# Performance work log

Measured on AMD Instinct MI355X. Metric: run time of the kernel, lower is better.

The kernel has to match this reference:

```python
import jax, jax.numpy as jnp
import numpy as np

N_NODES = 50000
N_RAND_EDGES = 800000
IN_FEATS = 128
NUM_HEADS = 4
OUT_FEATS = 32
NEG_SLOPE = 0.2


def setup_inputs() -> dict:
    key = jax.random.key(0)
    k_feat, k_src, k_dst, k_w, k_al, k_ar, k_b = jax.random.split(key, 7)
    feat = jax.random.normal(k_feat, (N_NODES, IN_FEATS), dtype=jnp.float32)
    # random edges + self-loops so every node has in-degree >= 1 (DGL requirement)
    src_r = jax.random.randint(k_src, (N_RAND_EDGES,), 0, N_NODES)
    dst_r = jax.random.randint(k_dst, (N_RAND_EDGES,), 0, N_NODES)
    loops = jnp.arange(N_NODES, dtype=src_r.dtype)
    src = jnp.concatenate([src_r, loops]).astype(jnp.int64)
    dst = jnp.concatenate([dst_r, loops]).astype(jnp.int64)
    W = jax.random.normal(k_w, (NUM_HEADS * OUT_FEATS, IN_FEATS), dtype=jnp.float32) * 0.05
    attn_l = jax.random.normal(k_al, (1, NUM_HEADS, OUT_FEATS), dtype=jnp.float32) * 0.1
    attn_r = jax.random.normal(k_ar, (1, NUM_HEADS, OUT_FEATS), dtype=jnp.float32) * 0.1
    bias = jnp.zeros((NUM_HEADS * OUT_FEATS,), dtype=jnp.float32)
    return {"feat": feat, "src": src, "dst": dst, "W": W,
            "attn_l": attn_l, "attn_r": attn_r, "bias": bias}


def _gat_forward(feat, src, dst, W, attn_l, attn_r, bias):
    n = feat.shape[0]
    # shared projection: in homogeneous path feat_src2 = feat_dst2 = fc(h)
    ft = (feat @ W.T).reshape(n, NUM_HEADS, OUT_FEATS)       # [N,H,D]
    el = jnp.sum(ft * attn_l, axis=-1)                        # [N,H]
    er = jnp.sum(ft * attn_r, axis=-1)                        # [N,H]
    e = el[src] + er[dst]                                     # [E,H]
    e = jnp.where(e > 0, e, NEG_SLOPE * e)                    # leaky_relu
    # edge softmax per destination node (numerically stable)
    m = jax.ops.segment_max(e, dst, num_segments=n)           # [N,H]
    ex = jnp.exp(e - m[dst])
    s = jax.ops.segment_sum(ex, dst, num_segments=n)          # [N,H]
    a = ex / s[dst]                                           # [E,H]
    # u_mul_e -> sum : attention-weighted aggregation
    msg1 = ft[src] * a[:, :, None]                            # [E,H,D]
    initial_ft = jax.ops.segment_sum(msg1, dst, num_segments=n)
    # u_mul_v -> sum : elementwise src*dst product aggregation
    msg2 = ft[src] * ft[dst]                                  # [E,H,D]
    add_ft = jax.ops.segment_sum(msg2, dst, num_segments=n)
    rst = initial_ft + add_ft + bias.reshape(1, NUM_HEADS, OUT_FEATS)
    return rst


def reference(feat, src, dst, W, attn_l, attn_r, bias):
    return _gat_forward(feat, src, dst, W, attn_l, attn_r, bias)
```

## Files before the change

kernel.cpp:

```cpp
#include <hip/hip_runtime.h>
#include <hip/hip_bf16.h>

#define IN_FEATS 128
#define HD 128
#define NEG_SLOPE 0.2f
#define LDR 128
#define CAP 64

typedef short s8v __attribute__((ext_vector_type(8)));
typedef float f4v __attribute__((ext_vector_type(4)));

static __device__ __forceinline__ unsigned short f2bf(float f) {
    unsigned int u = __float_as_uint(f);
    unsigned int r = (u + 0x7FFFu + ((u >> 16) & 1u)) >> 16;
    return (unsigned short)r;
}
static __device__ __forceinline__ float bf2f(unsigned short h) {
    return __uint_as_float(((unsigned int)h) << 16);
}

#define GM 64
#define LDA 136
#define SCAT_BLOCKS 512
__global__ __launch_bounds__(256) void scatter_gemm(const float* __restrict__ feat,
                                                    const float* __restrict__ W,
                                                    const float* __restrict__ attn_l,
                                                    const float* __restrict__ attn_r,
                                                    const int* __restrict__ src,
                                                    const int* __restrict__ dst,
                                                    int* __restrict__ cnt,
                                                    int* __restrict__ bucket, int E,
                                                    unsigned short* __restrict__ ftb,
                                                    float* __restrict__ el,
                                                    float* __restrict__ er, int N) {
    if (blockIdx.x < SCAT_BLOCKS) {
        const int gstride = SCAT_BLOCKS * 256;
        for (int i = blockIdx.x * 256 + threadIdx.x; i < E; i += gstride) {
            int d = dst[i];
            int pos = atomicAdd(&cnt[d], 1);
            if (pos < CAP) bucket[((size_t)d << 6) + pos] = src[i];
        }
        return;
    }

    __shared__ unsigned short Wb[128][LDA];
    __shared__ unsigned short Ab[GM][LDA];

    const int tid   = threadIdx.x;
    const int wave  = tid >> 6;
    const int lane  = tid & 63;
    const int m     = lane & 15;
    const int quad  = lane >> 4;
    const int rbase = (blockIdx.x - SCAT_BLOCKS) * GM;

    const float4* W4 = (const float4*)W;
    for (int i = tid; i < 4096; i += 256) {
        int r = i >> 5, q = i & 31;
        float4 w = W4[i];
        ushort4 o;
        o.x = f2bf(w.x); o.y = f2bf(w.y); o.z = f2bf(w.z); o.w = f2bf(w.w);
        *(ushort4*)&Wb[r][q * 4] = o;
    }
    const float4* F4 = (const float4*)feat;
    for (int i = tid; i < 2048; i += 256) {
        int r = i >> 5, q = i & 31;
        int gr = rbase + r;
        float4 v = (gr < N) ? F4[(size_t)gr * 32 + q]
                            : make_float4(0.f, 0.f, 0.f, 0.f);
        ushort4 o;
        o.x = f2bf(v.x); o.y = f2bf(v.y); o.z = f2bf(v.z); o.w = f2bf(v.w);
        *(ushort4*)&Ab[r][q * 4] = o;
    }
    __syncthreads();

    f4v acc[8];
#pragma unroll
    for (int t = 0; t < 8; ++t) acc[t] = (f4v){0.f, 0.f, 0.f, 0.f};

    const int arow = wave * 16 + m;
#pragma unroll
    for (int k0 = 0; k0 < 4; ++k0) {
        s8v a = *(const s8v*)&Ab[arow][k0 * 32 + quad * 8];
#pragma unroll
        for (int t = 0; t < 8; ++t) {
            s8v b = *(const s8v*)&Wb[t * 16 + m][k0 * 32 + quad * 8];
            acc[t] = __builtin_amdgcn_mfma_f32_16x16x32_bf16(a, b, acc[t], 0, 0, 0);
        }
    }

#pragma unroll
    for (int reg = 0; reg < 4; ++reg) {
        int gr = rbase + wave * 16 + quad * 4 + reg;
        if (gr < N) {
            unsigned short* dstrow = &ftb[(size_t)gr * LDR];
#pragma unroll
            for (int t = 0; t < 8; ++t)
                dstrow[t * 16 + m] = f2bf(acc[t][reg]);
        }
    }

    float al[8], ar[8];
#pragma unroll
    for (int t = 0; t < 8; ++t) {
        al[t] = attn_l[t * 16 + m];
        ar[t] = attn_r[t * 16 + m];
    }
#pragma unroll
    for (int h = 0; h < 4; ++h) {
#pragma unroll
        for (int reg = 0; reg < 4; ++reg) {
            float pl = acc[2 * h][reg] * al[2 * h] + acc[2 * h + 1][reg] * al[2 * h + 1];
            float pr = acc[2 * h][reg] * ar[2 * h] + acc[2 * h + 1][reg] * ar[2 * h + 1];
            pl += __shfl_xor(pl, 1); pr += __shfl_xor(pr, 1);
            pl += __shfl_xor(pl, 2); pr += __shfl_xor(pr, 2);
            pl += __shfl_xor(pl, 4); pr += __shfl_xor(pr, 4);
            pl += __shfl_xor(pl, 8); pr += __shfl_xor(pr, 8);
            if (m == 0) {
                int gr = rbase + wave * 16 + quad * 4 + reg;
                if (gr < N) {
                    el[gr * 4 + h] = pl;
                    er[gr * 4 + h] = pr;
                }
            }
        }
    }
}

__global__ __launch_bounds__(256) void aggregate_kernel(
        const unsigned short* __restrict__ ftb, const float* __restrict__ el,
        const float* __restrict__ er, const int* __restrict__ cnt,
        const int* __restrict__ bucket, const float* __restrict__ bias,
        float* __restrict__ out, int N) {
    const int n    = (blockIdx.x * blockDim.x + threadIdx.x) >> 6;
    const int lane = threadIdx.x & 63;
    if (n >= N) return;
    const int h  = lane >> 4;
    const int c0 = lane * 2;

    const float ern = er[(n << 2) + h];
    ushort2 tn = *(const ushort2*)(ftb + (size_t)n * LDR + c0);
    const float ftn0 = bf2f(tn.x), ftn1 = bf2f(tn.y);

    int deg = min(cnt[n], CAP);
    const int* eb = bucket + ((size_t)n << 6);

    float a0 = 0.f, a1 = 0.f;
    float b0 = 0.f, b1 = 0.f;
    float sum = 0.f;

    int i = 0;
    for (; i + 4 <= deg; i += 4) {
        int sA = eb[i + 0], sB = eb[i + 1], sC = eb[i + 2], sD = eb[i + 3];
        float eA = el[(sA << 2) + h];
        float eB = el[(sB << 2) + h];
        float eC = el[(sC << 2) + h];
        float eD = el[(sD << 2) + h];
        ushort2 fA = *(const ushort2*)(ftb + (size_t)sA * LDR + c0);
        ushort2 fB = *(const ushort2*)(ftb + (size_t)sB * LDR + c0);
        ushort2 fC = *(const ushort2*)(ftb + (size_t)sC * LDR + c0);
        ushort2 fD = *(const ushort2*)(ftb + (size_t)sD * LDR + c0);
        eA += ern; eB += ern; eC += ern; eD += ern;
        eA = eA > 0.f ? eA : NEG_SLOPE * eA;
        eB = eB > 0.f ? eB : NEG_SLOPE * eB;
        eC = eC > 0.f ? eC : NEG_SLOPE * eC;
        eD = eD > 0.f ? eD : NEG_SLOPE * eD;
        float xA = __expf(eA), xB = __expf(eB);
        float xC = __expf(eC), xD = __expf(eD);
        float fAx = bf2f(fA.x), fAy = bf2f(fA.y);
        float fBx = bf2f(fB.x), fBy = bf2f(fB.y);
        float fCx = bf2f(fC.x), fCy = bf2f(fC.y);
        float fDx = bf2f(fD.x), fDy = bf2f(fD.y);
        sum += (xA + xB) + (xC + xD);
        a0 += xA * fAx + xB * fBx + xC * fCx + xD * fDx;
        a1 += xA * fAy + xB * fBy + xC * fCy + xD * fDy;
        b0 += (fAx + fBx) + (fCx + fDx);
        b1 += (fAy + fBy) + (fCy + fDy);
    }
    for (; i < deg; ++i) {
        int s = eb[i];
        float e = el[(s << 2) + h] + ern;
        e = e > 0.f ? e : NEG_SLOPE * e;
        float x = __expf(e);
        ushort2 f = *(const ushort2*)(ftb + (size_t)s * LDR + c0);
        float fx = bf2f(f.x), fy = bf2f(f.y);
        sum += x;
        a0 += x * fx; a1 += x * fy;
        b0 += fx;     b1 += fy;
    }

    float inv = 1.f / sum;
    float2 o;
    o.x = a0 * inv + ftn0 * b0 + bias[c0];
    o.y = a1 * inv + ftn1 * b1 + bias[c0 + 1];
    *(float2*)(out + (size_t)n * HD + c0) = o;
}

extern "C" void kernel_launch(void* const* d_in, const int* in_sizes, int n_in,
                              void* d_out, int out_size, void* d_ws, size_t ws_size,
                              hipStream_t stream) {
    const float* feat   = (const float*)d_in[0];
    const int*   src    = (const int*)d_in[1];
    const int*   dst    = (const int*)d_in[2];
    const float* W      = (const float*)d_in[3];
    const float* attn_l = (const float*)d_in[4];
    const float* attn_r = (const float*)d_in[5];
    const float* bias   = (const float*)d_in[6];

    const int N = in_sizes[0] / IN_FEATS;
    const int E = in_sizes[1];

    char* p = (char*)d_ws;
    auto alloc = [&](size_t bytes) {
        char* q = p;
        p += (bytes + 255) & ~(size_t)255;
        return q;
    };
    unsigned short* ftb = (unsigned short*)alloc((size_t)N * LDR * 2);
    float* el    = (float*)alloc((size_t)N * 4 * 4);
    float* er    = (float*)alloc((size_t)N * 4 * 4);
    int*   cnt   = (int*)alloc((size_t)N * 4);
    int*   bucket= (int*)alloc((size_t)N * CAP * 4);

    hipMemsetAsync(cnt, 0, (size_t)N * 4, stream);

    const int gemm_blocks = (N + GM - 1) / GM;
    scatter_gemm<<<SCAT_BLOCKS + gemm_blocks, 256, 0, stream>>>(
        feat, W, attn_l, attn_r, src, dst, cnt, bucket, E, ftb, el, er, N);

    long long threads = (long long)N * 64;
    int agg_blocks = (int)((threads + 255) / 256);
    aggregate_kernel<<<agg_blocks, 256, 0, stream>>>(ftb, el, er, cnt, bucket,
                                                     bias, (float*)d_out, N);
}
```

Before: 195.7 us.

## Load W fragments directly from global, pack bf16 pairs, unroll scatter by two

```diff
diff --git a/kernel.cpp b/kernel.cpp
--- a/kernel.cpp
+++ b/kernel.cpp
@@ -17,6 +17,10 @@
 }
 static __device__ __forceinline__ float bf2f(unsigned short h) {
     return __uint_as_float(((unsigned int)h) << 16);
+}
+static __device__ __forceinline__ unsigned int pk2(float x, float y) {
+    __hip_bfloat162 h = __float22bfloat162_rn(make_float2(x, y));
+    return *(unsigned int*)&h;
 }
 
 #define GM 64
@@ -35,15 +39,20 @@
                                                     float* __restrict__ er, int N) {
     if (blockIdx.x < SCAT_BLOCKS) {
         const int gstride = SCAT_BLOCKS * 256;
-        for (int i = blockIdx.x * 256 + threadIdx.x; i < E; i += gstride) {
-            int d = dst[i];
-            int pos = atomicAdd(&cnt[d], 1);
-            if (pos < CAP) bucket[((size_t)d << 6) + pos] = src[i];
+        for (int i = blockIdx.x * 256 + threadIdx.x; i < E; i += 2 * gstride) {
+            int j = i + gstride;
+            int d0 = dst[i];
+            int s0 = src[i];
+            bool hasj = (j < E);
+            int d1 = hasj ? dst[j] : 0;
+            int p0 = atomicAdd(&cnt[d0], 1);
+            int p1 = hasj ? atomicAdd(&cnt[d1], 1) : CAP;
+            if (p0 < CAP) bucket[((size_t)d0 << 6) + p0] = s0;
+            if (hasj && p1 < CAP) bucket[((size_t)d1 << 6) + p1] = src[j];
         }
         return;
     }
 
-    __shared__ unsigned short Wb[128][LDA];
     __shared__ unsigned short Ab[GM][LDA];
 
     const int tid   = threadIdx.x;
@@ -53,14 +62,6 @@
     const int quad  = lane >> 4;
     const int rbase = (blockIdx.x - SCAT_BLOCKS) * GM;
 
-    const float4* W4 = (const float4*)W;
-    for (int i = tid; i < 4096; i += 256) {
-        int r = i >> 5, q = i & 31;
-        float4 w = W4[i];
-        ushort4 o;
-        o.x = f2bf(w.x); o.y = f2bf(w.y); o.z = f2bf(w.z); o.w = f2bf(w.w);
-        *(ushort4*)&Wb[r][q * 4] = o;
-    }
     const float4* F4 = (const float4*)feat;
     for (int i = tid; i < 2048; i += 256) {
         int r = i >> 5, q = i & 31;
@@ -68,7 +69,9 @@
         float4 v = (gr < N) ? F4[(size_t)gr * 32 + q]
                             : make_float4(0.f, 0.f, 0.f, 0.f);
         ushort4 o;
-        o.x = f2bf(v.x); o.y = f2bf(v.y); o.z = f2bf(v.z); o.w = f2bf(v.w);
+        unsigned int u0 = pk2(v.x, v.y), u1 = pk2(v.z, v.w);
+        o.x = (unsigned short)(u0 & 0xFFFF); o.y = (unsigned short)(u0 >> 16);
+        o.z = (unsigned short)(u1 & 0xFFFF); o.w = (unsigned short)(u1 >> 16);
         *(ushort4*)&Ab[r][q * 4] = o;
     }
     __syncthreads();
@@ -77,14 +80,22 @@
 #pragma unroll
     for (int t = 0; t < 8; ++t) acc[t] = (f4v){0.f, 0.f, 0.f, 0.f};
 
+    const float4* W4 = (const float4*)W;
     const int arow = wave * 16 + m;
 #pragma unroll
     for (int k0 = 0; k0 < 4; ++k0) {
         s8v a = *(const s8v*)&Ab[arow][k0 * 32 + quad * 8];
 #pragma unroll
         for (int t = 0; t < 8; ++t) {
-            s8v b = *(const s8v*)&Wb[t * 16 + m][k0 * 32 + quad * 8];
-            acc[t] = __builtin_amdgcn_mfma_f32_16x16x32_bf16(a, b, acc[t], 0, 0, 0);
+            int col = t * 16 + m;
+            float4 w0 = W4[col * 32 + k0 * 8 + quad * 2 + 0];
+            float4 w1 = W4[col * 32 + k0 * 8 + quad * 2 + 1];
+            union { s8v v; unsigned int u[4]; } b;
+            b.u[0] = pk2(w0.x, w0.y);
+            b.u[1] = pk2(w0.z, w0.w);
+            b.u[2] = pk2(w1.x, w1.y);
+            b.u[3] = pk2(w1.z, w1.w);
+            acc[t] = __builtin_amdgcn_mfma_f32_16x16x32_bf16(a, b.v, acc[t], 0, 0, 0);
         }
     }
 
```

Result: slower. 208.7 us (+6.7%).
